# Performance work log

Hardware: AMD Instinct MI355X
Metric: run time of the kernel (lower is better)

The kernel has to match this reference:

```python
import math
import jax, jax.numpy as jnp
import numpy as np

D_MODEL = 1024
D_HIDDEN = 2048
N_EXPERTS = 8
TOP_K = 2
CAPACITY_FACTOR = 1.25


def setup_inputs() -> dict:
    key = jax.random.key(0)
    k0, k1, k2, k3 = jax.random.split(key, 4)
    B, T = 2, 2048
    x = jax.random.normal(k0, (B, T, D_MODEL), dtype=jnp.float32)
    # torch nn.Linear stores weight as [out_features, in_features]
    w_router = jax.random.normal(k1, (N_EXPERTS, D_MODEL), dtype=jnp.float32) * 0.02
    w_gate = jax.random.normal(k2, (D_HIDDEN, D_MODEL), dtype=jnp.float32) * 0.02
    w_down = jax.random.normal(k3, (N_EXPERTS, D_MODEL, D_HIDDEN), dtype=jnp.float32) * 0.02
    return {"x": x, "w_router": w_router, "w_gate": w_gate, "w_down": w_down}


def _moe_forward(x, w_router, w_gate, w_down):
    B, T, D = x.shape
    N = B * T
    xf = x.reshape(N, D)

    # Router (computed in fp32, as in the original)
    logits = xf.astype(jnp.float32) @ w_router.T            # [N, E]
    gates = jax.nn.softmax(logits, axis=-1)                  # [N, E]
    topk_gates, topk_idx = jax.lax.top_k(gates, TOP_K)       # [N, K]

    # expert_mask[n, e] = 1 if expert e is among token n's top-k
    expert_mask = jax.nn.one_hot(topk_idx, N_EXPERTS, dtype=jnp.int32).sum(axis=1)  # [N, E]

    # Capacity masking via cumulative position within each expert's buffer
    capacity = math.ceil(N / N_EXPERTS * CAPACITY_FACTOR)
    position_in_expert = jnp.cumsum(expert_mask, axis=0) - 1
    expert_mask = expert_mask * (position_in_expert < capacity)

    keep = jnp.take_along_axis(expert_mask, topk_idx, axis=1) > 0  # [N, K]
    topk_gates = topk_gates * keep
    topk_gates = topk_gates / (topk_gates.sum(axis=-1, keepdims=True) + 1e-6)

    # Shared up-projection + SiLU (dropout = 0)
    hidden = jax.nn.silu(xf @ w_gate.T)                      # [N, H]

    # combine[n, e] = sum_k topk_gates[n, k] * [topk_idx[n, k] == e]
    combine = (topk_gates[:, :, None]
               * jax.nn.one_hot(topk_idx, N_EXPERTS, dtype=topk_gates.dtype)).sum(axis=1)  # [N, E]

    # Combine: y[n] = sum_e combine[n, e] * (hidden[n] @ w_down[e].T)
    # (dropped tokens have combine weight 0, matching the gated index_add in torch)
    y = jnp.zeros((N, D), dtype=x.dtype)
    for e in range(N_EXPERTS):  # small fixed loop over experts
        y = y + combine[:, e:e + 1] * (hidden @ w_down[e].T)
    return y.reshape(B, T, D)


def reference(x, w_router, w_gate, w_down):
    return _moe_forward(x, w_router, w_gate, w_down)
```

## Files before the change

kernel.cpp:

```cpp
#include <hip/hip_runtime.h>
#include <hip/hip_bf16.h>
#include <math.h>

#define NTOK 4096
#define DMODEL 1024
#define DHID 2048
#define NEXP 8
#define CAP 640

typedef __attribute__((ext_vector_type(8))) short short8;
typedef __attribute__((ext_vector_type(4))) float f32x4;

__device__ inline short f2bf(float f) {
    union { float f; unsigned u; } v; v.f = f;
    unsigned r = v.u + 0x7FFF + ((v.u >> 16) & 1);
    return (short)(r >> 16);
}
__device__ inline float bf2f(unsigned short u) {
    union { unsigned u; float f; } v; v.u = ((unsigned)u) << 16; return v.f;
}
__device__ inline void async16(const short* g, short* l) {
    __builtin_amdgcn_global_load_lds(
        (const __attribute__((address_space(1))) unsigned*)g,
        (__attribute__((address_space(3))) unsigned*)l, 16, 0, 0);
}

__global__ __launch_bounds__(256) void router_kernel(
        const float* __restrict__ x, const float* __restrict__ wr, short* __restrict__ Xb,
        int2* __restrict__ topk_idx, float2* __restrict__ topk_gate)
{
    const int token = blockIdx.x * 4 + (threadIdx.x >> 6);
    const int lane  = threadIdx.x & 63;
    const float* xr = x + (size_t)token * DMODEL + lane * 16;
    float4 xv[4];
#pragma unroll
    for (int j = 0; j < 4; j++) xv[j] = ((const float4*)xr)[j];
    short8 s0 = { f2bf(xv[0].x), f2bf(xv[0].y), f2bf(xv[0].z), f2bf(xv[0].w),
                  f2bf(xv[1].x), f2bf(xv[1].y), f2bf(xv[1].z), f2bf(xv[1].w) };
    short8 s1 = { f2bf(xv[2].x), f2bf(xv[2].y), f2bf(xv[2].z), f2bf(xv[2].w),
                  f2bf(xv[3].x), f2bf(xv[3].y), f2bf(xv[3].z), f2bf(xv[3].w) };
    short* xo = Xb + (size_t)token * DMODEL + lane * 16;
    *(short8*)xo = s0;
    *(short8*)(xo + 8) = s1;

    float acc[NEXP];
#pragma unroll
    for (int e = 0; e < NEXP; e++) acc[e] = 0.f;
#pragma unroll
    for (int j = 0; j < 4; j++) {
#pragma unroll
        for (int e = 0; e < NEXP; e++) {
            float4 wv = ((const float4*)(wr + e * DMODEL + lane * 16))[j];
            acc[e] += xv[j].x * wv.x + xv[j].y * wv.y + xv[j].z * wv.z + xv[j].w * wv.w;
        }
    }
#pragma unroll
    for (int off = 32; off >= 1; off >>= 1) {
#pragma unroll
        for (int e = 0; e < NEXP; e++) acc[e] += __shfl_xor(acc[e], off, 64);
    }
    if (lane == 0) {
        float m = acc[0];
#pragma unroll
        for (int e = 1; e < NEXP; e++) m = fmaxf(m, acc[e]);
        float den = 0.f, g[NEXP];
#pragma unroll
        for (int e = 0; e < NEXP; e++) { g[e] = __expf(acc[e] - m); den += g[e]; }
        float inv = 1.f / den;
#pragma unroll
        for (int e = 0; e < NEXP; e++) g[e] *= inv;
        int i0 = 0; float l0 = acc[0];
#pragma unroll
        for (int e = 1; e < NEXP; e++) if (acc[e] > l0) { l0 = acc[e]; i0 = e; }
        int i1 = -1; float l1 = -1e30f;
#pragma unroll
        for (int e = 0; e < NEXP; e++) if (e != i0 && acc[e] > l1) { l1 = acc[e]; i1 = e; }
        topk_idx[token]  = make_int2(i0, i1);
        topk_gate[token] = make_float2(g[i0], g[i1]);
    }
}

__global__ __launch_bounds__(256) void router_fb_kernel(
        const float* __restrict__ x, const float* __restrict__ wr,
        int2* __restrict__ topk_idx, float2* __restrict__ topk_gate)
{
    const int token = blockIdx.x * 4 + (threadIdx.x >> 6);
    const int lane  = threadIdx.x & 63;
    const float* xr = x + (size_t)token * DMODEL + lane * 16;
    float acc[NEXP];
#pragma unroll
    for (int e = 0; e < NEXP; e++) acc[e] = 0.f;
#pragma unroll
    for (int j = 0; j < 4; j++) {
        float4 xv = ((const float4*)xr)[j];
#pragma unroll
        for (int e = 0; e < NEXP; e++) {
            float4 wv = ((const float4*)(wr + e * DMODEL + lane * 16))[j];
            acc[e] += xv.x * wv.x + xv.y * wv.y + xv.z * wv.z + xv.w * wv.w;
        }
    }
#pragma unroll
    for (int off = 32; off >= 1; off >>= 1) {
#pragma unroll
        for (int e = 0; e < NEXP; e++) acc[e] += __shfl_xor(acc[e], off, 64);
    }
    if (lane == 0) {
        float m = acc[0];
#pragma unroll
        for (int e = 1; e < NEXP; e++) m = fmaxf(m, acc[e]);
        float den = 0.f, g[NEXP];
#pragma unroll
        for (int e = 0; e < NEXP; e++) { g[e] = __expf(acc[e] - m); den += g[e]; }
        float inv = 1.f / den;
#pragma unroll
        for (int e = 0; e < NEXP; e++) g[e] *= inv;
        int i0 = 0; float l0 = acc[0];
#pragma unroll
        for (int e = 1; e < NEXP; e++) if (acc[e] > l0) { l0 = acc[e]; i0 = e; }
        int i1 = -1; float l1 = -1e30f;
#pragma unroll
        for (int e = 0; e < NEXP; e++) if (e != i0 && acc[e] > l1) { l1 = acc[e]; i1 = e; }
        topk_idx[token]  = make_int2(i0, i1);
        topk_gate[token] = make_float2(g[i0], g[i1]);
    }
}

__global__ __launch_bounds__(256) void convert_kernel(
        const float* __restrict__ src, short* __restrict__ dst)
{
    const size_t base = ((size_t)blockIdx.x * 256 + threadIdx.x) * 8;
    float4 a = ((const float4*)(src + base))[0];
    float4 b = ((const float4*)(src + base))[1];
    short8 s = { f2bf(a.x), f2bf(a.y), f2bf(a.z), f2bf(a.w),
                 f2bf(b.x), f2bf(b.y), f2bf(b.z), f2bf(b.w) };
    *(short8*)(dst + base) = s;
}

__global__ __launch_bounds__(1024) void scan_kernel(
        const int2* __restrict__ topk_idx, const float2* __restrict__ topk_gate,
        int* __restrict__ gtok, float* __restrict__ gw, int* __restrict__ gcnt,
        int2* __restrict__ tslot, float2* __restrict__ tw)
{
    __shared__ unsigned long long wt0[16], wt1[16];
    const int th = threadIdx.x, lane = th & 63, wid = th >> 6;
    int2 idx[4]; float2 gt[4];
#pragma unroll
    for (int j = 0; j < 4; j++) { idx[j] = topk_idx[th * 4 + j]; gt[j] = topk_gate[th * 4 + j]; }
    unsigned long long c0 = 0, c1 = 0;
#pragma unroll
    for (int j = 0; j < 4; j++) {
        int e0 = idx[j].x, e1 = idx[j].y;
        if (e0 < 4) c0 += 1ull << (e0 * 16); else c1 += 1ull << ((e0 - 4) * 16);
        if (e1 < 4) c0 += 1ull << (e1 * 16); else c1 += 1ull << ((e1 - 4) * 16);
    }
    const unsigned long long my0 = c0, my1 = c1;
#pragma unroll
    for (int d = 1; d < 64; d <<= 1) {
        unsigned long long t0 = __shfl_up(c0, d, 64);
        unsigned long long t1 = __shfl_up(c1, d, 64);
        if (lane >= d) { c0 += t0; c1 += t1; }
    }
    if (lane == 63) { wt0[wid] = c0; wt1[wid] = c1; }
    __syncthreads();
    unsigned long long o0 = 0, o1 = 0;
    for (int w = 0; w < wid; w++) { o0 += wt0[w]; o1 += wt1[w]; }
    c0 += o0; c1 += o1;
    if (th == 1023) {
#pragma unroll
        for (int e = 0; e < 4; e++) gcnt[e]     = min((int)((c0 >> (e * 16)) & 0xFFFF), CAP);
#pragma unroll
        for (int e = 0; e < 4; e++) gcnt[4 + e] = min((int)((c1 >> (e * 16)) & 0xFFFF), CAP);
    }
    const unsigned long long x0 = c0 - my0, x1 = c1 - my1;
    int base[NEXP];
#pragma unroll
    for (int e = 0; e < 4; e++) base[e]     = (int)((x0 >> (e * 16)) & 0xFFFF);
#pragma unroll
    for (int e = 0; e < 4; e++) base[4 + e] = (int)((x1 >> (e * 16)) & 0xFFFF);
#pragma unroll
    for (int j = 0; j < 4; j++) {
        const int n = th * 4 + j;
        const int e0 = idx[j].x, e1 = idx[j].y;
        const int p0 = base[e0]++;
        const int p1 = base[e1]++;
        const bool k0 = p0 < CAP, k1 = p1 < CAP;
        const float gg0 = k0 ? gt[j].x : 0.f, gg1 = k1 ? gt[j].y : 0.f;
        const float invs = 1.f / (gg0 + gg1 + 1e-6f);
        const int s0 = k0 ? e0 * CAP + p0 : 0;
        const int s1 = k1 ? e1 * CAP + p1 : 0;
        if (k0) { gtok[s0] = n; gw[s0] = gg0 * invs; }
        if (k1) { gtok[s1] = n; gw[s1] = gg1 * invs; }
        tslot[n] = make_int2(s0, s1);
        tw[n]    = make_float2(gg0 * invs, gg1 * invs);
    }
}

__global__ __launch_bounds__(256) void gemm1_kernel(
        const short* __restrict__ Xb, const short* __restrict__ WGb, short* __restrict__ Hid)
{
    __shared__ __align__(16) short As[128 * 64];
    __shared__ __align__(16) short Bs[128 * 64];
    const int t = threadIdx.x;
    const int wave = t >> 6, lane = t & 63;
    const int m0 = blockIdx.y * 128, n0 = blockIdx.x * 128;
    const int wm = (wave >> 1) * 64, wn = (wave & 1) * 64;
    const int lm = lane & 15, lq = lane >> 4;

    const short *ga[4], *gb[4];
    short *la[4], *lb[4];
#pragma unroll
    for (int j = 0; j < 4; j++) {
        const int b   = wave * 4 + j;
        const int row = (b >> 1) * 16 + lm;
        const int col = (b & 1) * 32 + lq * 8;
        la[j] = &As[b * 512 + lane * 8];
        lb[j] = &Bs[b * 512 + lane * 8];
        ga[j] = Xb  + (size_t)(m0 + row) * DMODEL + col;
        gb[j] = WGb + (size_t)(n0 + row) * DMODEL + col;
    }

    f32x4 acc[4][4];
#pragma unroll
    for (int a = 0; a < 4; a++)
#pragma unroll
        for (int b = 0; b < 4; b++) acc[a][b] = (f32x4)(0.f);

    for (int k0 = 0; k0 < DMODEL; k0 += 64) {
#pragma unroll
        for (int j = 0; j < 4; j++) { async16(ga[j] + k0, la[j]); async16(gb[j] + k0, lb[j]); }
        __syncthreads();
#pragma unroll
        for (int kk = 0; kk < 2; kk++) {
            short8 af[4], bf[4];
#pragma unroll
            for (int mi = 0; mi < 4; mi++)
                af[mi] = *(const short8*)&As[((((wm >> 4) + mi) * 2 + kk) * 64 + lane) * 8];
#pragma unroll
            for (int ni = 0; ni < 4; ni++)
                bf[ni] = *(const short8*)&Bs[((((wn >> 4) + ni) * 2 + kk) * 64 + lane) * 8];
#pragma unroll
            for (int mi = 0; mi < 4; mi++)
#pragma unroll
                for (int ni = 0; ni < 4; ni++)
                    acc[mi][ni] = __builtin_amdgcn_mfma_f32_16x16x32_bf16(af[mi], bf[ni], acc[mi][ni], 0, 0, 0);
        }
        __syncthreads();
    }
#pragma unroll
    for (int mi = 0; mi < 4; mi++)
#pragma unroll
        for (int i = 0; i < 4; i++) {
            const int row = m0 + wm + mi * 16 + lq * 4 + i;
#pragma unroll
            for (int ni = 0; ni < 4; ni++) {
                const int col = n0 + wn + ni * 16 + lm;
                const float v = acc[mi][ni][i];
                const float s = v / (1.f + __expf(-v));
                Hid[(size_t)row * DHID + col] = f2bf(s);
            }
        }
}

__global__ __launch_bounds__(256) void gemm2_kernel(
        const short* __restrict__ Hid, const short* __restrict__ WDb,
        const int* __restrict__ gtok, const int* __restrict__ gcnt,
        short* __restrict__ Yp)
{
    __shared__ __align__(16) short As[128 * 64];
    __shared__ __align__(16) short Bs[128 * 64];
    __shared__ int tok_s[128];
    const int e  = blockIdx.x;
    const int n0 = blockIdx.y * 128;
    const int m0 = blockIdx.z * 128;
    const int cnt = gcnt[e];
    if (m0 >= cnt) return;
    const int t = threadIdx.x;
    const int wave = t >> 6, lane = t & 63;
    const int wm = (wave >> 1) * 64, wn = (wave & 1) * 64;
    const int lm = lane & 15, lq = lane >> 4;
    const short* WDe = WDb + (size_t)e * DMODEL * DHID;

    if (t < 128) {
        const int r = m0 + t;
        tok_s[t] = (r < cnt) ? gtok[e * CAP + r] : 0;
    }
    __syncthreads();

    const short *ga[4], *gb[4];
    short *la[4], *lb[4];
#pragma unroll
    for (int j = 0; j < 4; j++) {
        const int b   = wave * 4 + j;
        const int row = (b >> 1) * 16 + lm;
        const int col = (b & 1) * 32 + lq * 8;
        la[j] = &As[b * 512 + lane * 8];
        lb[j] = &Bs[b * 512 + lane * 8];
        ga[j] = Hid + (size_t)tok_s[row] * DHID + col;
        gb[j] = WDe + (size_t)(n0 + row) * DHID + col;
    }

    f32x4 acc[4][4];
#pragma unroll
    for (int a = 0; a < 4; a++)
#pragma unroll
        for (int b = 0; b < 4; b++) acc[a][b] = (f32x4)(0.f);

    for (int k0 = 0; k0 < DHID; k0 += 64) {
#pragma unroll
        for (int j = 0; j < 4; j++) { async16(ga[j] + k0, la[j]); async16(gb[j] + k0, lb[j]); }
        __syncthreads();
#pragma unroll
        for (int kk = 0; kk < 2; kk++) {
            short8 af[4], bf[4];
#pragma unroll
            for (int mi = 0; mi < 4; mi++)
                af[mi] = *(const short8*)&As[((((wm >> 4) + mi) * 2 + kk) * 64 + lane) * 8];
#pragma unroll
            for (int ni = 0; ni < 4; ni++)
                bf[ni] = *(const short8*)&Bs[((((wn >> 4) + ni) * 2 + kk) * 64 + lane) * 8];
#pragma unroll
            for (int mi = 0; mi < 4; mi++)
#pragma unroll
                for (int ni = 0; ni < 4; ni++)
                    acc[mi][ni] = __builtin_amdgcn_mfma_f32_16x16x32_bf16(af[mi], bf[ni], acc[mi][ni], 0, 0, 0);
        }
        __syncthreads();
    }
#pragma unroll
    for (int mi = 0; mi < 4; mi++)
#pragma unroll
        for (int i = 0; i < 4; i++) {
            const int slot = e * CAP + m0 + wm + mi * 16 + lq * 4 + i;
#pragma unroll
            for (int ni = 0; ni < 4; ni++) {
                const int col = n0 + wn + ni * 16 + lm;
                Yp[(size_t)slot * DMODEL + col] = f2bf(acc[mi][ni][i]);
            }
        }
}

__global__ __launch_bounds__(256) void combine_kernel(
        const short* __restrict__ Yp, const int2* __restrict__ tslot,
        const float2* __restrict__ tw, float* __restrict__ y)
{
    const int token = blockIdx.x;
    const int c = threadIdx.x * 4;
    const int2   s = tslot[token];
    const float2 w = tw[token];
    ushort4 a = *(const ushort4*)((const unsigned short*)Yp + (size_t)s.x * DMODEL + c);
    ushort4 b = *(const ushort4*)((const unsigned short*)Yp + (size_t)s.y * DMODEL + c);
    float4 o;
    o.x = w.x * bf2f(a.x) + w.y * bf2f(b.x);
    o.y = w.x * bf2f(a.y) + w.y * bf2f(b.y);
    o.z = w.x * bf2f(a.z) + w.y * bf2f(b.z);
    o.w = w.x * bf2f(a.w) + w.y * bf2f(b.w);
    *(float4*)&y[(size_t)token * DMODEL + c] = o;
}

__global__ __launch_bounds__(256) void gemm1_fb_kernel(
        const float* __restrict__ X, const float* __restrict__ WG, short* __restrict__ Hid)
{
    __shared__ short As[128][72];
    __shared__ short Bs[128][72];
    const int t = threadIdx.x;
    const int wave = t >> 6, lane = t & 63;
    const int m0 = blockIdx.y * 128, n0 = blockIdx.x * 128;
    const int wm = (wave >> 1) * 64, wn = (wave & 1) * 64;
    const int lm = lane & 15, lq = lane >> 4, lk = lq * 8;
    const int r0 = t >> 3, c8 = (t & 7) * 8;

    f32x4 acc[4][4];
#pragma unroll
    for (int a = 0; a < 4; a++)
#pragma unroll
        for (int b = 0; b < 4; b++) acc[a][b] = (f32x4)(0.f);

    for (int k0 = 0; k0 < DMODEL; k0 += 64) {
#pragma unroll
        for (int i = 0; i < 4; i++) {
            const int row = r0 + i * 32;
            const float* ga = X + (size_t)(m0 + row) * DMODEL + k0 + c8;
            float4 v0 = ((const float4*)ga)[0];
            float4 v1 = ((const float4*)ga)[1];
            short8 s = { f2bf(v0.x), f2bf(v0.y), f2bf(v0.z), f2bf(v0.w),
                         f2bf(v1.x), f2bf(v1.y), f2bf(v1.z), f2bf(v1.w) };
            *(short8*)&As[row][c8] = s;
            const float* gb = WG + (size_t)(n0 + row) * DMODEL + k0 + c8;
            float4 w0 = ((const float4*)gb)[0];
            float4 w1 = ((const float4*)gb)[1];
            short8 sw = { f2bf(w0.x), f2bf(w0.y), f2bf(w0.z), f2bf(w0.w),
                          f2bf(w1.x), f2bf(w1.y), f2bf(w1.z), f2bf(w1.w) };
            *(short8*)&Bs[row][c8] = sw;
        }
        __syncthreads();
#pragma unroll
        for (int kk = 0; kk < 64; kk += 32) {
            short8 af[4], bf[4];
#pragma unroll
            for (int mi = 0; mi < 4; mi++) af[mi] = *(const short8*)&As[wm + mi * 16 + lm][kk + lk];
#pragma unroll
            for (int ni = 0; ni < 4; ni++) bf[ni] = *(const short8*)&Bs[wn + ni * 16 + lm][kk + lk];
#pragma unroll
            for (int mi = 0; mi < 4; mi++)
#pragma unroll
                for (int ni = 0; ni < 4; ni++)
                    acc[mi][ni] = __builtin_amdgcn_mfma_f32_16x16x32_bf16(af[mi], bf[ni], acc[mi][ni], 0, 0, 0);
        }
        __syncthreads();
    }
#pragma unroll
    for (int mi = 0; mi < 4; mi++)
#pragma unroll
        for (int i = 0; i < 4; i++) {
            const int row = m0 + wm + mi * 16 + lq * 4 + i;
#pragma unroll
            for (int ni = 0; ni < 4; ni++) {
                const int col = n0 + wn + ni * 16 + lm;
                const float v = acc[mi][ni][i];
                const float s = v / (1.f + __expf(-v));
                Hid[(size_t)row * DHID + col] = f2bf(s);
            }
        }
}

__global__ __launch_bounds__(256) void gemm2_fb_kernel(
        const short* __restrict__ Hid, const float* __restrict__ WD,
        const int* __restrict__ gtok, const float* __restrict__ gw,
        const int* __restrict__ gcnt, float* __restrict__ Y)
{
    __shared__ short As[128][72];
    __shared__ short Bs[128][72];
    __shared__ int   tok_s[128];
    __shared__ float w_s[128];
    const int e = blockIdx.z;
    const int cnt = gcnt[e];
    const int m0 = blockIdx.y * 128;
    if (m0 >= cnt) return;
    const int n0 = blockIdx.x * 128;
    const int t = threadIdx.x;
    const int wave = t >> 6, lane = t & 63;
    const int wm = (wave >> 1) * 64, wn = (wave & 1) * 64;
    const int lm = lane & 15, lq = lane >> 4, lk = lq * 8;
    const int r0 = t >> 3, c8 = (t & 7) * 8;
    const float* WDe = WD + (size_t)e * DMODEL * DHID;

    if (t < 128) {
        const int r = m0 + t;
        const bool v = r < cnt;
        tok_s[t] = v ? gtok[e * CAP + r] : 0;
        w_s[t]   = v ? gw[e * CAP + r] : 0.f;
    }
    __syncthreads();

    f32x4 acc[4][4];
#pragma unroll
    for (int a = 0; a < 4; a++)
#pragma unroll
        for (int b = 0; b < 4; b++) acc[a][b] = (f32x4)(0.f);

    const int tokA[4] = { tok_s[r0], tok_s[r0 + 32], tok_s[r0 + 64], tok_s[r0 + 96] };

    for (int k0 = 0; k0 < DHID; k0 += 64) {
#pragma unroll
        for (int i = 0; i < 4; i++) {
            const int row = r0 + i * 32;
            uint4 av = *(const uint4*)(Hid + (size_t)tokA[i] * DHID + k0 + c8);
            *(uint4*)&As[row][c8] = av;
            const float* gb = WDe + (size_t)(n0 + row) * DHID + k0 + c8;
            float4 w0 = ((const float4*)gb)[0];
            float4 w1 = ((const float4*)gb)[1];
            short8 sw = { f2bf(w0.x), f2bf(w0.y), f2bf(w0.z), f2bf(w0.w),
                          f2bf(w1.x), f2bf(w1.y), f2bf(w1.z), f2bf(w1.w) };
            *(short8*)&Bs[row][c8] = sw;
        }
        __syncthreads();
#pragma unroll
        for (int kk = 0; kk < 64; kk += 32) {
            short8 af[4], bf[4];
#pragma unroll
            for (int mi = 0; mi < 4; mi++) af[mi] = *(const short8*)&As[wm + mi * 16 + lm][kk + lk];
#pragma unroll
            for (int ni = 0; ni < 4; ni++) bf[ni] = *(const short8*)&Bs[wn + ni * 16 + lm][kk + lk];
#pragma unroll
            for (int mi = 0; mi < 4; mi++)
#pragma unroll
                for (int ni = 0; ni < 4; ni++)
                    acc[mi][ni] = __builtin_amdgcn_mfma_f32_16x16x32_bf16(af[mi], bf[ni], acc[mi][ni], 0, 0, 0);
        }
        __syncthreads();
    }
#pragma unroll
    for (int mi = 0; mi < 4; mi++)
#pragma unroll
        for (int i = 0; i < 4; i++) {
            const int r = wm + mi * 16 + lq * 4 + i;
            const float wr = w_s[r];
            if (wr > 0.f) {
                const int token = tok_s[r];
#pragma unroll
                for (int ni = 0; ni < 4; ni++) {
                    const int col = n0 + wn + ni * 16 + lm;
                    atomicAdd(&Y[(size_t)token * DMODEL + col], acc[mi][ni][i] * wr);
                }
            }
        }
}

extern "C" void kernel_launch(void* const* d_in, const int* in_sizes, int n_in,
                              void* d_out, int out_size, void* d_ws, size_t ws_size,
                              hipStream_t stream) {
    const float* x  = (const float*)d_in[0];
    const float* wr = (const float*)d_in[1];
    const float* wg = (const float*)d_in[2];
    const float* wd = (const float*)d_in[3];
    float* y = (float*)d_out;

    char* w = (char*)d_ws;
    int2*   topk_idx  = (int2*)w;    w += NTOK * sizeof(int2);
    float2* topk_gate = (float2*)w;  w += NTOK * sizeof(float2);
    int*    gtok      = (int*)w;     w += NEXP * CAP * sizeof(int);
    float*  gw        = (float*)w;   w += NEXP * CAP * sizeof(float);
    int*    gcnt      = (int*)w;     w += 256;
    int2*   tslot     = (int2*)w;    w += NTOK * sizeof(int2);
    float2* tw        = (float2*)w;  w += NTOK * sizeof(float2);
    short*  Hid       = (short*)w;   w += (size_t)NTOK * DHID * sizeof(short);
    short*  WDb       = (short*)w;   w += (size_t)NEXP * DMODEL * DHID * sizeof(short);
    short*  Xb        = (short*)w;
    short*  WGb       = (short*)(w + (size_t)NTOK * DMODEL * sizeof(short));
    short*  Yp        = (short*)w;
    w += (size_t)NTOK * DMODEL * sizeof(short) + (size_t)DHID * DMODEL * sizeof(short);
    const size_t need_full = (size_t)(w - (char*)d_ws);

    if (ws_size >= need_full) {
        router_kernel<<<NTOK / 4, 256, 0, stream>>>(x, wr, Xb, topk_idx, topk_gate);
        convert_kernel<<<(DHID * DMODEL) / (256 * 8), 256, 0, stream>>>(wg, WGb);
        scan_kernel<<<1, 1024, 0, stream>>>(topk_idx, topk_gate, gtok, gw, gcnt, tslot, tw);
        gemm1_kernel<<<dim3(DHID / 128, NTOK / 128), 256, 0, stream>>>(Xb, WGb, Hid);
        convert_kernel<<<(NEXP * DMODEL * DHID) / (256 * 8), 256, 0, stream>>>(wd, WDb);
        gemm2_kernel<<<dim3(NEXP, DMODEL / 128, CAP / 128), 256, 0, stream>>>(
            Hid, WDb, gtok, gcnt, Yp);
        combine_kernel<<<NTOK, 256, 0, stream>>>(Yp, tslot, tw, y);
    } else {
        hipMemsetAsync(y, 0, (size_t)NTOK * DMODEL * sizeof(float), stream);
        router_fb_kernel<<<NTOK / 4, 256, 0, stream>>>(x, wr, topk_idx, topk_gate);
        scan_kernel<<<1, 1024, 0, stream>>>(topk_idx, topk_gate, gtok, gw, gcnt, tslot, tw);
        gemm1_fb_kernel<<<dim3(DHID / 128, NTOK / 128), 256, 0, stream>>>(x, wg, Hid);
        gemm2_fb_kernel<<<dim3(DMODEL / 128, (CAP + 127) / 128, NEXP), 256, 0, stream>>>(
            Hid, wd, gtok, gw, gcnt, y);
    }
}
```

Before: 247.9 us.

## Double-buffer LDS tiles in both GEMMs and merge weight conversions into one launch

Both bf16 MFMA GEMM kernels now use two LDS buffers per operand and prefetch the next K-tile with async global-to-LDS loads while computing the current one. Explicit vmcnt/lgkmcnt waits and raw barriers replace __syncthreads. The two fp32-to-bf16 weight conversion launches are merged into a single kernel covering both weight tensors, removing one launch. The changes aim to hide global load latency behind MFMA work, at the cost of doubling LDS per block (about 64KB), which may reduce occupancy.

New measurement: 245.2 us. No clear change (-1.1%).

```diff
diff --git a/kernel.cpp b/kernel.cpp
--- a/kernel.cpp
+++ b/kernel.cpp
@@ -24,6 +24,10 @@
         (const __attribute__((address_space(1))) unsigned*)g,
         (__attribute__((address_space(3))) unsigned*)l, 16, 0, 0);
 }
+#define WAIT_VM8()   __builtin_amdgcn_s_waitcnt(0xF78)
+#define WAIT_VM0()   __builtin_amdgcn_s_waitcnt(0xF70)
+#define WAIT_LGKM0() __builtin_amdgcn_s_waitcnt(0xC07F)
+#define BARRIER()    __builtin_amdgcn_s_barrier()
 
 __global__ __launch_bounds__(256) void router_kernel(
         const float* __restrict__ x, const float* __restrict__ wr, short* __restrict__ Xb,
@@ -125,15 +129,19 @@
     }
 }
 
-__global__ __launch_bounds__(256) void convert_kernel(
-        const float* __restrict__ src, short* __restrict__ dst)
-{
-    const size_t base = ((size_t)blockIdx.x * 256 + threadIdx.x) * 8;
-    float4 a = ((const float4*)(src + base))[0];
-    float4 b = ((const float4*)(src + base))[1];
-    short8 s = { f2bf(a.x), f2bf(a.y), f2bf(a.z), f2bf(a.w),
-                 f2bf(b.x), f2bf(b.y), f2bf(b.z), f2bf(b.w) };
-    *(short8*)(dst + base) = s;
+__global__ __launch_bounds__(256) void convert2_kernel(
+        const float* __restrict__ a, short* __restrict__ da, size_t na,
+        const float* __restrict__ b, short* __restrict__ db)
+{
+    size_t i = ((size_t)blockIdx.x * 256 + threadIdx.x) * 8;
+    const float* src; short* dst;
+    if (i < na) { src = a + i; dst = da + i; }
+    else        { src = b + (i - na); dst = db + (i - na); }
+    float4 v0 = ((const float4*)src)[0];
+    float4 v1 = ((const float4*)src)[1];
+    short8 s = { f2bf(v0.x), f2bf(v0.y), f2bf(v0.z), f2bf(v0.w),
+                 f2bf(v1.x), f2bf(v1.y), f2bf(v1.z), f2bf(v1.w) };
+    *(short8*)dst = s;
 }
 
 __global__ __launch_bounds__(1024) void scan_kernel(
@@ -198,8 +206,8 @@
 __global__ __launch_bounds__(256) void gemm1_kernel(
         const short* __restrict__ Xb, const short* __restrict__ WGb, short* __restrict__ Hid)
 {
-    __shared__ __align__(16) short As[128 * 64];
-    __shared__ __align__(16) short Bs[128 * 64];
+    __shared__ __align__(16) short As[2][128 * 64];
+    __shared__ __align__(16) short Bs[2][128 * 64];
     const int t = threadIdx.x;
     const int wave = t >> 6, lane = t & 63;
     const int m0 = blockIdx.y * 128, n0 = blockIdx.x * 128;
@@ -207,14 +215,13 @@
     const int lm = lane & 15, lq = lane >> 4;
 
     const short *ga[4], *gb[4];
-    short *la[4], *lb[4];
+    int loff[4];
 #pragma unroll
     for (int j = 0; j < 4; j++) {
         const int b   = wave * 4 + j;
         const int row = (b >> 1) * 16 + lm;
         const int col = (b & 1) * 32 + lq * 8;
-        la[j] = &As[b * 512 + lane * 8];
-        lb[j] = &Bs[b * 512 + lane * 8];
+        loff[j] = b * 512 + lane * 8;
         ga[j] = Xb  + (size_t)(m0 + row) * DMODEL + col;
         gb[j] = WGb + (size_t)(n0 + row) * DMODEL + col;
     }
@@ -225,26 +232,38 @@
 #pragma unroll
         for (int b = 0; b < 4; b++) acc[a][b] = (f32x4)(0.f);
 
+#pragma unroll
+    for (int j = 0; j < 4; j++) { async16(ga[j], &As[0][loff[j]]); async16(gb[j], &Bs[0][loff[j]]); }
+
     for (int k0 = 0; k0 < DMODEL; k0 += 64) {
-#pragma unroll
-        for (int j = 0; j < 4; j++) { async16(ga[j] + k0, la[j]); async16(gb[j] + k0, lb[j]); }
-        __syncthreads();
+        const int cur = (k0 >> 6) & 1;
+        const int nxt = cur ^ 1;
+        const int k1 = k0 + 64;
+        if (k1 < DMODEL) {
+#pragma unroll
+            for (int j = 0; j < 4; j++) { async16(ga[j] + k1, &As[nxt][loff[j]]); async16(gb[j] + k1, &Bs[nxt][loff[j]]); }
+            WAIT_VM8();
+        } else {
+            WAIT_VM0();
+        }
+        BARRIER();
 #pragma unroll
         for (int kk = 0; kk < 2; kk++) {
             short8 af[4], bf[4];
 #pragma unroll
             for (int mi = 0; mi < 4; mi++)
-                af[mi] = *(const short8*)&As[((((wm >> 4) + mi) * 2 + kk) * 64 + lane) * 8];
+                af[mi] = *(const short8*)&As[cur][((((wm >> 4) + mi) * 2 + kk) * 64 + lane) * 8];
 #pragma unroll
             for (int ni = 0; ni < 4; ni++)
-                bf[ni] = *(const short8*)&Bs[((((wn >> 4) + ni) * 2 + kk) * 64 + lane) * 8];
+                bf[ni] = *(const short8*)&Bs[cur][((((wn >> 4) + ni) * 2 + kk) * 64 + lane) * 8];
 #pragma unroll
             for (int mi = 0; mi < 4; mi++)
 #pragma unroll
                 for (int ni = 0; ni < 4; ni++)
                     acc[mi][ni] = __builtin_amdgcn_mfma_f32_16x16x32_bf16(af[mi], bf[ni], acc[mi][ni], 0, 0, 0);
         }
-        __syncthreads();
+        WAIT_LGKM0();
+        BARRIER();
     }
 #pragma unroll
     for (int mi = 0; mi < 4; mi++)
@@ -266,8 +285,8 @@
         const int* __restrict__ gtok, const int* __restrict__ gcnt,
         short* __restrict__ Yp)
 {
-    __shared__ __align__(16) short As[128 * 64];
-    __shared__ __align__(16) short Bs[128 * 64];
+    __shared__ __align__(16) short As[2][128 * 64];
+    __shared__ __align__(16) short Bs[2][128 * 64];
     __shared__ int tok_s[128];
     const int e  = blockIdx.x;
     const int n0 = blockIdx.y * 128;
@@ -280,21 +299,17 @@
     const int lm = lane & 15, lq = lane >> 4;
     const short* WDe = WDb + (size_t)e * DMODEL * DHID;
 
-    if (t < 128) {
-        const int r = m0 + t;
-        tok_s[t] = (r < cnt) ? gtok[e * CAP + r] : 0;
-    }
+    if (t < 128) tok_s[t] = (m0 + t < cnt) ? gtok[e * CAP + m0 + t] : 0;
     __syncthreads();
 
     const short *ga[4], *gb[4];
-    short *la[4], *lb[4];
+    int loff[4];
 #pragma unroll
     for (int j = 0; j < 4; j++) {
         const int b   = wave * 4 + j;
         const int row = (b >> 1) * 16 + lm;
         const int col = (b & 1) * 32 + lq * 8;
-        la[j] = &As[b * 512 + lane * 8];
-        lb[j] = &Bs[b * 512 + lane * 8];
+        loff[j] = b * 512 + lane * 8;
         ga[j] = Hid + (size_t)tok_s[row] * DHID + col;
         gb[j] = WDe + (size_t)(n0 + row) * DHID + col;
     }
@@ -305,26 +320,38 @@
 #pragma unroll
         for (int b = 0; b < 4; b++) acc[a][b] = (f32x4)(0.f);
 
+#pragma unroll
+    for (int j = 0; j < 4; j++) { async16(ga[j], &As[0][loff[j]]); async16(gb[j], &Bs[0][loff[j]]); }
+
     for (int k0 = 0; k0 < DHID; k0 += 64) {
-#pragma unroll
-        for (int j = 0; j < 4; j++) { async16(ga[j] + k0, la[j]); async16(gb[j] + k0, lb[j]); }
-        __syncthreads();
+        const int cur = (k0 >> 6) & 1;
+        const int nxt = cur ^ 1;
+        const int k1 = k0 + 64;
+        if (k1 < DHID) {
+#pragma unroll
+            for (int j = 0; j < 4; j++) { async16(ga[j] + k1, &As[nxt][loff[j]]); async16(gb[j] + k1, &Bs[nxt][loff[j]]); }
+            WAIT_VM8();
+        } else {
+            WAIT_VM0();
+        }
+        BARRIER();
 #pragma unroll
         for (int kk = 0; kk < 2; kk++) {
             short8 af[4], bf[4];
 #pragma unroll
             for (int mi = 0; mi < 4; mi++)
-                af[mi] = *(const short8*)&As[((((wm >> 4) + mi) * 2 + kk) * 64 + lane) * 8];
+                af[mi] = *(const short8*)&As[cur][((((wm >> 4) + mi) * 2 + kk) * 64 + lane) * 8];
 #pragma unroll
             for (int ni = 0; ni < 4; ni++)
-                bf[ni] = *(const short8*)&Bs[((((wn >> 4) + ni) * 2 + kk) * 64 + lane) * 8];
+                bf[ni] = *(const short8*)&Bs[cur][((((wn >> 4) + ni) * 2 + kk) * 64 + lane) * 8];
 #pragma unroll
             for (int mi = 0; mi < 4; mi++)
 #pragma unroll
                 for (int ni = 0; ni < 4; ni++)
                     acc[mi][ni] = __builtin_amdgcn_mfma_f32_16x16x32_bf16(af[mi], bf[ni], acc[mi][ni], 0, 0, 0);
         }
-        __syncthreads();
+        WAIT_LGKM0();
+        BARRIER();
     }
 #pragma unroll
     for (int mi = 0; mi < 4; mi++)
@@ -533,10 +560,10 @@
 
     if (ws_size >= need_full) {
         router_kernel<<<NTOK / 4, 256, 0, stream>>>(x, wr, Xb, topk_idx, topk_gate);
-        convert_kernel<<<(DHID * DMODEL) / (256 * 8), 256, 0, stream>>>(wg, WGb);
+        convert2_kernel<<<(DHID * DMODEL + NEXP * DMODEL * DHID) / (256 * 8), 256, 0, stream>>>(
+            wg, WGb, (size_t)DHID * DMODEL, wd, WDb);
         scan_kernel<<<1, 1024, 0, stream>>>(topk_idx, topk_gate, gtok, gw, gcnt, tslot, tw);
         gemm1_kernel<<<dim3(DHID / 128, NTOK / 128), 256, 0, stream>>>(Xb, WGb, Hid);
-        convert_kernel<<<(NEXP * DMODEL * DHID) / (256 * 8), 256, 0, stream>>>(wd, WDb);
         gemm2_kernel<<<dim3(NEXP, DMODEL / 128, CAP / 128), 256, 0, stream>>>(
             Hid, WDb, gtok, gcnt, Yp);
         combine_kernel<<<NTOK, 256, 0, stream>>>(Yp, tslot, tw, y);
```

## Shrink GEMM tiles to 128x64 with two waves and fuse weight conversions

Applied to the files above, without the earlier changes.

Both GEMM kernels move from 128x128 tiles with four waves to 128x64 tiles with two waves, each wave owning a 64x64 sub-tile. This doubles the block count so the device is filled more evenly, especially for the expert GEMM. The cost is lower arithmetic intensity per block and more global-to-LDS loads per thread. The two fp32-to-bf16 weight conversion launches are also merged into one kernel, saving a launch at the price of a per-thread branch.

Result: slower. 267.0 us (+7.7%).

```diff
diff --git a/kernel.cpp b/kernel.cpp
--- a/kernel.cpp
+++ b/kernel.cpp
@@ -125,15 +125,19 @@
     }
 }
 
-__global__ __launch_bounds__(256) void convert_kernel(
-        const float* __restrict__ src, short* __restrict__ dst)
-{
-    const size_t base = ((size_t)blockIdx.x * 256 + threadIdx.x) * 8;
-    float4 a = ((const float4*)(src + base))[0];
-    float4 b = ((const float4*)(src + base))[1];
-    short8 s = { f2bf(a.x), f2bf(a.y), f2bf(a.z), f2bf(a.w),
-                 f2bf(b.x), f2bf(b.y), f2bf(b.z), f2bf(b.w) };
-    *(short8*)(dst + base) = s;
+__global__ __launch_bounds__(256) void convert2_kernel(
+        const float* __restrict__ a, short* __restrict__ da, size_t na,
+        const float* __restrict__ b, short* __restrict__ db)
+{
+    size_t i = ((size_t)blockIdx.x * 256 + threadIdx.x) * 8;
+    const float* src; short* dst;
+    if (i < na) { src = a + i; dst = da + i; }
+    else        { src = b + (i - na); dst = db + (i - na); }
+    float4 v0 = ((const float4*)src)[0];
+    float4 v1 = ((const float4*)src)[1];
+    short8 s = { f2bf(v0.x), f2bf(v0.y), f2bf(v0.z), f2bf(v0.w),
+                 f2bf(v1.x), f2bf(v1.y), f2bf(v1.z), f2bf(v1.w) };
+    *(short8*)dst = s;
 }
 
 __global__ __launch_bounds__(1024) void scan_kernel(
@@ -195,28 +199,34 @@
     }
 }
 
-__global__ __launch_bounds__(256) void gemm1_kernel(
+__global__ __launch_bounds__(128) void gemm1_kernel(
         const short* __restrict__ Xb, const short* __restrict__ WGb, short* __restrict__ Hid)
 {
     __shared__ __align__(16) short As[128 * 64];
-    __shared__ __align__(16) short Bs[128 * 64];
+    __shared__ __align__(16) short Bs[64 * 64];
     const int t = threadIdx.x;
     const int wave = t >> 6, lane = t & 63;
-    const int m0 = blockIdx.y * 128, n0 = blockIdx.x * 128;
-    const int wm = (wave >> 1) * 64, wn = (wave & 1) * 64;
+    const int m0 = blockIdx.y * 128, n0 = blockIdx.x * 64;
     const int lm = lane & 15, lq = lane >> 4;
 
-    const short *ga[4], *gb[4];
-    short *la[4], *lb[4];
-#pragma unroll
-    for (int j = 0; j < 4; j++) {
-        const int b   = wave * 4 + j;
-        const int row = (b >> 1) * 16 + lm;
-        const int col = (b & 1) * 32 + lq * 8;
-        la[j] = &As[b * 512 + lane * 8];
-        lb[j] = &Bs[b * 512 + lane * 8];
-        ga[j] = Xb  + (size_t)(m0 + row) * DMODEL + col;
-        gb[j] = WGb + (size_t)(n0 + row) * DMODEL + col;
+    const short *ga[12]; short* la[12];
+#pragma unroll
+    for (int j = 0; j < 12; j++) {
+        const int c = j * 128 + t;
+        if (c < 1024) {
+            const int b = c >> 6, l = c & 63;
+            const int row = (b >> 1) * 16 + (l & 15);
+            const int col = (b & 1) * 32 + (l >> 4) * 8;
+            la[j] = &As[c * 8];
+            ga[j] = Xb + (size_t)(m0 + row) * DMODEL + col;
+        } else {
+            const int cb = c - 1024;
+            const int b = cb >> 6, l = cb & 63;
+            const int row = (b >> 1) * 16 + (l & 15);
+            const int col = (b & 1) * 32 + (l >> 4) * 8;
+            la[j] = &Bs[cb * 8];
+            ga[j] = WGb + (size_t)(n0 + row) * DMODEL + col;
+        }
     }
 
     f32x4 acc[4][4];
@@ -227,17 +237,17 @@
 
     for (int k0 = 0; k0 < DMODEL; k0 += 64) {
 #pragma unroll
-        for (int j = 0; j < 4; j++) { async16(ga[j] + k0, la[j]); async16(gb[j] + k0, lb[j]); }
+        for (int j = 0; j < 12; j++) async16(ga[j] + k0, la[j]);
         __syncthreads();
 #pragma unroll
         for (int kk = 0; kk < 2; kk++) {
             short8 af[4], bf[4];
 #pragma unroll
             for (int mi = 0; mi < 4; mi++)
-                af[mi] = *(const short8*)&As[((((wm >> 4) + mi) * 2 + kk) * 64 + lane) * 8];
+                af[mi] = *(const short8*)&As[(((wave * 4 + mi) * 2 + kk) * 64 + lane) * 8];
 #pragma unroll
             for (int ni = 0; ni < 4; ni++)
-                bf[ni] = *(const short8*)&Bs[((((wn >> 4) + ni) * 2 + kk) * 64 + lane) * 8];
+                bf[ni] = *(const short8*)&Bs[((ni * 2 + kk) * 64 + lane) * 8];
 #pragma unroll
             for (int mi = 0; mi < 4; mi++)
 #pragma unroll
@@ -250,10 +260,10 @@
     for (int mi = 0; mi < 4; mi++)
 #pragma unroll
         for (int i = 0; i < 4; i++) {
-            const int row = m0 + wm + mi * 16 + lq * 4 + i;
+            const int row = m0 + wave * 64 + mi * 16 + lq * 4 + i;
 #pragma unroll
             for (int ni = 0; ni < 4; ni++) {
-                const int col = n0 + wn + ni * 16 + lm;
+                const int col = n0 + ni * 16 + lm;
                 const float v = acc[mi][ni][i];
                 const float s = v / (1.f + __expf(-v));
                 Hid[(size_t)row * DHID + col] = f2bf(s);
@@ -261,42 +271,45 @@
         }
 }
 
-__global__ __launch_bounds__(256) void gemm2_kernel(
+__global__ __launch_bounds__(128) void gemm2_kernel(
         const short* __restrict__ Hid, const short* __restrict__ WDb,
         const int* __restrict__ gtok, const int* __restrict__ gcnt,
         short* __restrict__ Yp)
 {
     __shared__ __align__(16) short As[128 * 64];
-    __shared__ __align__(16) short Bs[128 * 64];
+    __shared__ __align__(16) short Bs[64 * 64];
     __shared__ int tok_s[128];
     const int e  = blockIdx.x;
-    const int n0 = blockIdx.y * 128;
+    const int n0 = blockIdx.y * 64;
     const int m0 = blockIdx.z * 128;
     const int cnt = gcnt[e];
     if (m0 >= cnt) return;
     const int t = threadIdx.x;
     const int wave = t >> 6, lane = t & 63;
-    const int wm = (wave >> 1) * 64, wn = (wave & 1) * 64;
     const int lm = lane & 15, lq = lane >> 4;
     const short* WDe = WDb + (size_t)e * DMODEL * DHID;
 
-    if (t < 128) {
-        const int r = m0 + t;
-        tok_s[t] = (r < cnt) ? gtok[e * CAP + r] : 0;
-    }
+    tok_s[t] = (m0 + t < cnt) ? gtok[e * CAP + m0 + t] : 0;
     __syncthreads();
 
-    const short *ga[4], *gb[4];
-    short *la[4], *lb[4];
-#pragma unroll
-    for (int j = 0; j < 4; j++) {
-        const int b   = wave * 4 + j;
-        const int row = (b >> 1) * 16 + lm;
-        const int col = (b & 1) * 32 + lq * 8;
-        la[j] = &As[b * 512 + lane * 8];
-        lb[j] = &Bs[b * 512 + lane * 8];
-        ga[j] = Hid + (size_t)tok_s[row] * DHID + col;
-        gb[j] = WDe + (size_t)(n0 + row) * DHID + col;
+    const short *ga[12]; short* la[12];
+#pragma unroll
+    for (int j = 0; j < 12; j++) {
+        const int c = j * 128 + t;
+        if (c < 1024) {
+            const int b = c >> 6, l = c & 63;
+            const int row = (b >> 1) * 16 + (l & 15);
+            const int col = (b & 1) * 32 + (l >> 4) * 8;
+            la[j] = &As[c * 8];
+            ga[j] = Hid + (size_t)tok_s[row] * DHID + col;
+        } else {
+            const int cb = c - 1024;
+            const int b = cb >> 6, l = cb & 63;
+            const int row = (b >> 1) * 16 + (l & 15);
+            const int col = (b & 1) * 32 + (l >> 4) * 8;
+            la[j] = &Bs[cb * 8];
+            ga[j] = WDe + (size_t)(n0 + row) * DHID + col;
+        }
     }
 
     f32x4 acc[4][4];
@@ -307,17 +320,17 @@
 
     for (int k0 = 0; k0 < DHID; k0 += 64) {
 #pragma unroll
-        for (int j = 0; j < 4; j++) { async16(ga[j] + k0, la[j]); async16(gb[j] + k0, lb[j]); }
+        for (int j = 0; j < 12; j++) async16(ga[j] + k0, la[j]);
         __syncthreads();
 #pragma unroll
         for (int kk = 0; kk < 2; kk++) {
             short8 af[4], bf[4];
 #pragma unroll
             for (int mi = 0; mi < 4; mi++)
-                af[mi] = *(const short8*)&As[((((wm >> 4) + mi) * 2 + kk) * 64 + lane) * 8];
+                af[mi] = *(const short8*)&As[(((wave * 4 + mi) * 2 + kk) * 64 + lane) * 8];
 #pragma unroll
             for (int ni = 0; ni < 4; ni++)
-                bf[ni] = *(const short8*)&Bs[((((wn >> 4) + ni) * 2 + kk) * 64 + lane) * 8];
+                bf[ni] = *(const short8*)&Bs[((ni * 2 + kk) * 64 + lane) * 8];
 #pragma unroll
             for (int mi = 0; mi < 4; mi++)
 #pragma unroll
@@ -330,10 +343,10 @@
     for (int mi = 0; mi < 4; mi++)
 #pragma unroll
         for (int i = 0; i < 4; i++) {
-            const int slot = e * CAP + m0 + wm + mi * 16 + lq * 4 + i;
+            const int slot = e * CAP + m0 + wave * 64 + mi * 16 + lq * 4 + i;
 #pragma unroll
             for (int ni = 0; ni < 4; ni++) {
-                const int col = n0 + wn + ni * 16 + lm;
+                const int col = n0 + ni * 16 + lm;
                 Yp[(size_t)slot * DMODEL + col] = f2bf(acc[mi][ni][i]);
             }
         }
@@ -533,11 +546,11 @@
 
     if (ws_size >= need_full) {
         router_kernel<<<NTOK / 4, 256, 0, stream>>>(x, wr, Xb, topk_idx, topk_gate);
-        convert_kernel<<<(DHID * DMODEL) / (256 * 8), 256, 0, stream>>>(wg, WGb);
+        convert2_kernel<<<(DHID * DMODEL + NEXP * DMODEL * DHID) / (256 * 8), 256, 0, stream>>>(
+            wg, WGb, (size_t)DHID * DMODEL, wd, WDb);
         scan_kernel<<<1, 1024, 0, stream>>>(topk_idx, topk_gate, gtok, gw, gcnt, tslot, tw);
-        gemm1_kernel<<<dim3(DHID / 128, NTOK / 128), 256, 0, stream>>>(Xb, WGb, Hid);
-        convert_kernel<<<(NEXP * DMODEL * DHID) / (256 * 8), 256, 0, stream>>>(wd, WDb);
-        gemm2_kernel<<<dim3(NEXP, DMODEL / 128, CAP / 128), 256, 0, stream>>>(
+        gemm1_kernel<<<dim3(DHID / 64, NTOK / 128), 128, 0, stream>>>(Xb, WGb, Hid);
+        gemm2_kernel<<<dim3(NEXP, DMODEL / 64, CAP / 128), 128, 0, stream>>>(
             Hid, WDb, gtok, gcnt, Yp);
         combine_kernel<<<NTOK, 256, 0, stream>>>(Yp, tslot, tw, y);
     } else {
```

## Add split-K to both expert GEMMs and merge the two weight conversions

Applied to the files above, without the earlier changes.

Both GEMMs gain split-K. GEMM1 is split in two, writing bf16 partials to a new buffer that a separate kernel sums and passes through SiLU. GEMM2 is split in four, with the combine kernel summing the partials. The two fp32-to-bf16 weight conversions are merged into one launch. The aim is more blocks in flight to fill the CUs, since GEMM2 launches only 8x8x5 blocks, at the cost of extra partial-buffer traffic, an extra kernel, and rounding each partial to bf16 before it is summed.

New measurement: 249.1 us. Within noise of the previous version (+0.5%).

```diff
diff --git a/kernel.cpp b/kernel.cpp
--- a/kernel.cpp
+++ b/kernel.cpp
@@ -7,6 +7,7 @@
 #define DHID 2048
 #define NEXP 8
 #define CAP 640
+#define SLOTS (NEXP * CAP)
 
 typedef __attribute__((ext_vector_type(8))) short short8;
 typedef __attribute__((ext_vector_type(4))) float f32x4;
@@ -125,15 +126,19 @@
     }
 }
 
-__global__ __launch_bounds__(256) void convert_kernel(
-        const float* __restrict__ src, short* __restrict__ dst)
-{
-    const size_t base = ((size_t)blockIdx.x * 256 + threadIdx.x) * 8;
-    float4 a = ((const float4*)(src + base))[0];
-    float4 b = ((const float4*)(src + base))[1];
-    short8 s = { f2bf(a.x), f2bf(a.y), f2bf(a.z), f2bf(a.w),
-                 f2bf(b.x), f2bf(b.y), f2bf(b.z), f2bf(b.w) };
-    *(short8*)(dst + base) = s;
+__global__ __launch_bounds__(256) void convert2_kernel(
+        const float* __restrict__ a, short* __restrict__ da, size_t na,
+        const float* __restrict__ b, short* __restrict__ db)
+{
+    size_t i = ((size_t)blockIdx.x * 256 + threadIdx.x) * 8;
+    const float* src; short* dst;
+    if (i < na) { src = a + i; dst = da + i; }
+    else        { src = b + (i - na); dst = db + (i - na); }
+    float4 v0 = ((const float4*)src)[0];
+    float4 v1 = ((const float4*)src)[1];
+    short8 s = { f2bf(v0.x), f2bf(v0.y), f2bf(v0.z), f2bf(v0.w),
+                 f2bf(v1.x), f2bf(v1.y), f2bf(v1.z), f2bf(v1.w) };
+    *(short8*)dst = s;
 }
 
 __global__ __launch_bounds__(1024) void scan_kernel(
@@ -196,13 +201,15 @@
 }
 
 __global__ __launch_bounds__(256) void gemm1_kernel(
-        const short* __restrict__ Xb, const short* __restrict__ WGb, short* __restrict__ Hid)
+        const short* __restrict__ Xb, const short* __restrict__ WGb,
+        short* __restrict__ Hid, short* __restrict__ Hp, int KS)
 {
     __shared__ __align__(16) short As[128 * 64];
     __shared__ __align__(16) short Bs[128 * 64];
     const int t = threadIdx.x;
     const int wave = t >> 6, lane = t & 63;
-    const int m0 = blockIdx.y * 128, n0 = blockIdx.x * 128;
+    const int m0 = (blockIdx.y / KS) * 128, n0 = blockIdx.x * 128;
+    const int ks = blockIdx.y % KS;
     const int wm = (wave >> 1) * 64, wn = (wave & 1) * 64;
     const int lm = lane & 15, lq = lane >> 4;
 
@@ -225,7 +232,8 @@
 #pragma unroll
         for (int b = 0; b < 4; b++) acc[a][b] = (f32x4)(0.f);
 
-    for (int k0 = 0; k0 < DMODEL; k0 += 64) {
+    const int kbeg = ks * (DMODEL / KS), kend = kbeg + DMODEL / KS;
+    for (int k0 = kbeg; k0 < kend; k0 += 64) {
 #pragma unroll
         for (int j = 0; j < 4; j++) { async16(ga[j] + k0, la[j]); async16(gb[j] + k0, lb[j]); }
         __syncthreads();
@@ -246,32 +254,65 @@
         }
         __syncthreads();
     }
-#pragma unroll
-    for (int mi = 0; mi < 4; mi++)
-#pragma unroll
-        for (int i = 0; i < 4; i++) {
-            const int row = m0 + wm + mi * 16 + lq * 4 + i;
-#pragma unroll
-            for (int ni = 0; ni < 4; ni++) {
-                const int col = n0 + wn + ni * 16 + lm;
-                const float v = acc[mi][ni][i];
-                const float s = v / (1.f + __expf(-v));
-                Hid[(size_t)row * DHID + col] = f2bf(s);
+    if (KS == 1) {
+#pragma unroll
+        for (int mi = 0; mi < 4; mi++)
+#pragma unroll
+            for (int i = 0; i < 4; i++) {
+                const int row = m0 + wm + mi * 16 + lq * 4 + i;
+#pragma unroll
+                for (int ni = 0; ni < 4; ni++) {
+                    const int col = n0 + wn + ni * 16 + lm;
+                    const float v = acc[mi][ni][i];
+                    Hid[(size_t)row * DHID + col] = f2bf(v / (1.f + __expf(-v)));
+                }
             }
-        }
+    } else {
+        short* Ho = Hp + (size_t)ks * NTOK * DHID;
+#pragma unroll
+        for (int mi = 0; mi < 4; mi++)
+#pragma unroll
+            for (int i = 0; i < 4; i++) {
+                const int row = m0 + wm + mi * 16 + lq * 4 + i;
+#pragma unroll
+                for (int ni = 0; ni < 4; ni++) {
+                    const int col = n0 + wn + ni * 16 + lm;
+                    Ho[(size_t)row * DHID + col] = f2bf(acc[mi][ni][i]);
+                }
+            }
+    }
+}
+
+__global__ __launch_bounds__(256) void silu_merge_kernel(
+        const short* __restrict__ Hp, short* __restrict__ Hid)
+{
+    const size_t i = ((size_t)blockIdx.x * 256 + threadIdx.x) * 8;
+    const unsigned short* p0 = (const unsigned short*)Hp + i;
+    const unsigned short* p1 = (const unsigned short*)Hp + (size_t)NTOK * DHID + i;
+    ushort4 a0 = *(const ushort4*)p0, a1 = *(const ushort4*)(p0 + 4);
+    ushort4 b0 = *(const ushort4*)p1, b1 = *(const ushort4*)(p1 + 4);
+    float v[8] = { bf2f(a0.x) + bf2f(b0.x), bf2f(a0.y) + bf2f(b0.y),
+                   bf2f(a0.z) + bf2f(b0.z), bf2f(a0.w) + bf2f(b0.w),
+                   bf2f(a1.x) + bf2f(b1.x), bf2f(a1.y) + bf2f(b1.y),
+                   bf2f(a1.z) + bf2f(b1.z), bf2f(a1.w) + bf2f(b1.w) };
+    short8 o;
+#pragma unroll
+    for (int j = 0; j < 8; j++) o[j] = f2bf(v[j] / (1.f + __expf(-v[j])));
+    *(short8*)(Hid + i) = o;
 }
 
 __global__ __launch_bounds__(256) void gemm2_kernel(
         const short* __restrict__ Hid, const short* __restrict__ WDb,
         const int* __restrict__ gtok, const int* __restrict__ gcnt,
-        short* __restrict__ Yp)
+        short* __restrict__ Yp, int KS)
 {
     __shared__ __align__(16) short As[128 * 64];
     __shared__ __align__(16) short Bs[128 * 64];
     __shared__ int tok_s[128];
     const int e  = blockIdx.x;
     const int n0 = blockIdx.y * 128;
-    const int m0 = blockIdx.z * 128;
+    const int m0 = (blockIdx.z / KS) * 128;
+    const int ks = blockIdx.z % KS;
     const int cnt = gcnt[e];
     if (m0 >= cnt) return;
     const int t = threadIdx.x;
@@ -280,10 +321,7 @@
     const int lm = lane & 15, lq = lane >> 4;
     const short* WDe = WDb + (size_t)e * DMODEL * DHID;
 
-    if (t < 128) {
-        const int r = m0 + t;
-        tok_s[t] = (r < cnt) ? gtok[e * CAP + r] : 0;
-    }
+    if (t < 128) tok_s[t] = (m0 + t < cnt) ? gtok[e * CAP + m0 + t] : 0;
     __syncthreads();
 
     const short *ga[4], *gb[4];
@@ -305,7 +343,8 @@
 #pragma unroll
         for (int b = 0; b < 4; b++) acc[a][b] = (f32x4)(0.f);
 
-    for (int k0 = 0; k0 < DHID; k0 += 64) {
+    const int kbeg = ks * (DHID / KS), kend = kbeg + DHID / KS;
+    for (int k0 = kbeg; k0 < kend; k0 += 64) {
 #pragma unroll
         for (int j = 0; j < 4; j++) { async16(ga[j] + k0, la[j]); async16(gb[j] + k0, lb[j]); }
         __syncthreads();
@@ -326,6 +365,7 @@
         }
         __syncthreads();
     }
+    short* Yo = Yp + (size_t)ks * SLOTS * DMODEL;
 #pragma unroll
     for (int mi = 0; mi < 4; mi++)
 #pragma unroll
@@ -334,26 +374,29 @@
 #pragma unroll
             for (int ni = 0; ni < 4; ni++) {
                 const int col = n0 + wn + ni * 16 + lm;
-                Yp[(size_t)slot * DMODEL + col] = f2bf(acc[mi][ni][i]);
+                Yo[(size_t)slot * DMODEL + col] = f2bf(acc[mi][ni][i]);
             }
         }
 }
 
 __global__ __launch_bounds__(256) void combine_kernel(
         const short* __restrict__ Yp, const int2* __restrict__ tslot,
-        const float2* __restrict__ tw, float* __restrict__ y)
+        const float2* __restrict__ tw, float* __restrict__ y, int KS)
 {
     const int token = blockIdx.x;
     const int c = threadIdx.x * 4;
     const int2   s = tslot[token];
     const float2 w = tw[token];
-    ushort4 a = *(const ushort4*)((const unsigned short*)Yp + (size_t)s.x * DMODEL + c);
-    ushort4 b = *(const ushort4*)((const unsigned short*)Yp + (size_t)s.y * DMODEL + c);
-    float4 o;
-    o.x = w.x * bf2f(a.x) + w.y * bf2f(b.x);
-    o.y = w.x * bf2f(a.y) + w.y * bf2f(b.y);
-    o.z = w.x * bf2f(a.z) + w.y * bf2f(b.z);
-    o.w = w.x * bf2f(a.w) + w.y * bf2f(b.w);
+    float4 o = make_float4(0.f, 0.f, 0.f, 0.f);
+    for (int ks = 0; ks < KS; ks++) {
+        const unsigned short* base = (const unsigned short*)Yp + (size_t)ks * SLOTS * DMODEL;
+        ushort4 a = *(const ushort4*)(base + (size_t)s.x * DMODEL + c);
+        ushort4 b = *(const ushort4*)(base + (size_t)s.y * DMODEL + c);
+        o.x += w.x * bf2f(a.x) + w.y * bf2f(b.x);
+        o.y += w.x * bf2f(a.y) + w.y * bf2f(b.y);
+        o.z += w.x * bf2f(a.z) + w.y * bf2f(b.z);
+        o.w += w.x * bf2f(a.w) + w.y * bf2f(b.w);
+    }
     *(float4*)&y[(size_t)token * DMODEL + c] = o;
 }
 
@@ -528,18 +571,26 @@
     short*  Xb        = (short*)w;
     short*  WGb       = (short*)(w + (size_t)NTOK * DMODEL * sizeof(short));
     short*  Yp        = (short*)w;
-    w += (size_t)NTOK * DMODEL * sizeof(short) + (size_t)DHID * DMODEL * sizeof(short);
-    const size_t need_full = (size_t)(w - (char*)d_ws);
-
-    if (ws_size >= need_full) {
+    char*   w63       = w + ((size_t)NTOK * DMODEL + (size_t)DHID * DMODEL) * sizeof(short);
+    short*  Hp        = (short*)w63;
+    char*   w96       = w63 + (size_t)2 * NTOK * DHID * sizeof(short);
+    const size_t need63 = (size_t)(w63 - (char*)d_ws);
+    const size_t need96 = (size_t)(w96 - (char*)d_ws);
+
+    if (ws_size >= need63) {
+        const int KS1 = (ws_size >= need96) ? 2 : 1;
+        const int KS2 = (ws_size >= need96) ? 4 : 1;
         router_kernel<<<NTOK / 4, 256, 0, stream>>>(x, wr, Xb, topk_idx, topk_gate);
-        convert_kernel<<<(DHID * DMODEL) / (256 * 8), 256, 0, stream>>>(wg, WGb);
+        convert2_kernel<<<(DHID * DMODEL + NEXP * DMODEL * DHID) / (256 * 8), 256, 0, stream>>>(
+            wg, WGb, (size_t)DHID * DMODEL, wd, WDb);
         scan_kernel<<<1, 1024, 0, stream>>>(topk_idx, topk_gate, gtok, gw, gcnt, tslot, tw);
-        gemm1_kernel<<<dim3(DHID / 128, NTOK / 128), 256, 0, stream>>>(Xb, WGb, Hid);
-        convert_kernel<<<(NEXP * DMODEL * DHID) / (256 * 8), 256, 0, stream>>>(wd, WDb);
-        gemm2_kernel<<<dim3(NEXP, DMODEL / 128, CAP / 128), 256, 0, stream>>>(
-            Hid, WDb, gtok, gcnt, Yp);
-        combine_kernel<<<NTOK, 256, 0, stream>>>(Yp, tslot, tw, y);
+        gemm1_kernel<<<dim3(DHID / 128, (NTOK / 128) * KS1), 256, 0, stream>>>(
+            Xb, WGb, Hid, Hp, KS1);
+        if (KS1 == 2)
+            silu_merge_kernel<<<(NTOK * DHID) / (256 * 8), 256, 0, stream>>>(Hp, Hid);
+        gemm2_kernel<<<dim3(NEXP, DMODEL / 128, (CAP / 128) * KS2), 256, 0, stream>>>(
+            Hid, WDb, gtok, gcnt, Yp, KS2);
+        combine_kernel<<<NTOK, 256, 0, stream>>>(Yp, tslot, tw, y, KS2);
     } else {
         hipMemsetAsync(y, 0, (size_t)NTOK * DMODEL * sizeof(float), stream);
         router_fb_kernel<<<NTOK / 4, 256, 0, stream>>>(x, wr, topk_idx, topk_gate);
```
